# Kernel tuning notes

Measured on AMD Instinct MI355X. Metric: run time of the kernel, lower is better.

## Reference

```python
import jax, jax.numpy as jnp
import numpy as np

N_POINTS = 16
SPHERE_RADIUS = 2.5
BIG = 1e9

def _layernorm(x, g, b, eps=1e-5):
    mu = jnp.mean(x, axis=-1, keepdims=True)
    var = jnp.var(x, axis=-1, keepdims=True)
    return (x - mu) * jax.lax.rsqrt(var + eps) * g + b

def setup_inputs() -> dict:
    key = jax.random.key(0)
    ks = jax.random.split(key, 12)
    R, I, D, L = 1048576, 8, 64, 2
    orig = jax.random.normal(ks[0], (R, 3), jnp.float32)
    vec = jax.random.normal(ks[1], (R, 3), jnp.float32)
    vec = vec / jnp.linalg.norm(vec, axis=-1, keepdims=True)
    t1 = jax.random.uniform(ks[2], (I, R), jnp.float32) * 2.0
    t2 = t1 + jax.random.uniform(ks[3], (I, R), jnp.float32) * 0.5
    mask = jax.random.randint(ks[4], (I, R), 0, 2) > 0
    W_in = jax.random.normal(ks[5], (N_POINTS * 3, D), jnp.float32) * 0.1
    b_in = jnp.zeros((D,), jnp.float32)
    ln_g = jnp.ones((L, D), jnp.float32)
    ln_b = jnp.zeros((L, D), jnp.float32)
    W_mid = jax.random.normal(ks[6], (L, D, D), jnp.float32) * 0.1
    b_mid = jnp.zeros((L, D), jnp.float32)
    W_cls = jax.random.normal(ks[7], (D, 1), jnp.float32) * 0.1
    b_cls = jnp.zeros((1,), jnp.float32)
    W_dist = jax.random.normal(ks[8], (D, 1), jnp.float32) * 0.1
    b_dist = jnp.zeros((1,), jnp.float32)
    return dict(orig=orig, vec=vec, t1=t1, t2=t2, mask=mask,
                W_in=W_in, b_in=b_in, ln_g=ln_g, ln_b=ln_b,
                W_mid=W_mid, b_mid=b_mid, W_cls=W_cls, b_cls=b_cls,
                W_dist=W_dist, b_dist=b_dist)

def reference(orig, vec, t1, t2, mask, W_in, b_in, ln_g, ln_b, W_mid, b_mid,
              W_cls, b_cls, W_dist, b_dist):
    R = orig.shape[0]
    L = W_mid.shape[0]
    ts = jnp.linspace(0.0, 1.0, N_POINTS)  # [P]

    def net(x):  # x: [R, P*3]
        h = x @ W_in + b_in
        for l in range(L):
            h = jax.nn.relu(h)
            h = _layernorm(h, ln_g[l], ln_b[l])
            h = h @ W_mid[l] + b_mid[l]
        h = jax.nn.relu(h)
        cls = (h @ W_cls + b_cls)[:, 0]
        dval = (h @ W_dist + b_dist)[:, 0]
        return cls, dval

    def step(dist, it):
        m_i, t1_i, t2_i = it  # [R]
        dt = t2_i - t1_i
        inp_orig = orig + vec * t1_i[:, None]          # [R,3]
        inp_vec = vec * dt[:, None]                    # [R,3]
        # sample points along segment: [R, P, 3]
        inp = (inp_orig[:, None, :] + inp_vec[:, None, :] * ts[None, :, None]) / SPHERE_RADIUS
        cls, dval = net(inp.reshape(R, -1))
        dval = dval * dt + t1_i
        upd = (cls > 0) & (dval < dist) & m_i
        return jnp.where(upd, dval, dist), None

    dist0 = jnp.full((R,), BIG, jnp.float32)
    dist, _ = jax.lax.scan(step, dist0, (mask, t1, t2))
    dist = jnp.where(dist == BIG, 0.0, dist)
    return (dist > 0, dist)
```

## Files before the change

### kernel.cpp

```cpp
#include <hip/hip_runtime.h>
#include <math.h>

constexpr int   P      = 16;
constexpr int   DIN    = 48;
constexpr int   DH     = 64;
constexpr int   NITER  = 8;
constexpr int   NLAYER = 2;
constexpr float BIGV   = 1e9f;
constexpr float INV_R  = 1.0f / 2.5f;
constexpr int   RLOG   = 20;

typedef float f32x4 __attribute__((ext_vector_type(4)));
typedef const __attribute__((address_space(1))) f32x4 gf4_t;

__device__ __forceinline__ gf4_t* vmem(const float* p) {
    unsigned long long a = (unsigned long long)p;
    asm volatile("" : "+v"(a));
    return (gf4_t*)a;
}

__device__ __forceinline__ unsigned fkey(float f) {
    unsigned b = __float_as_uint(f);
    return (b & 0x80000000u) ? ~b : (b | 0x80000000u);
}
__device__ __forceinline__ float funkey(unsigned k) {
    unsigned b = (k & 0x80000000u) ? (k ^ 0x80000000u) : ~k;
    return __uint_as_float(b);
}

__device__ __noinline__
void slow_eval(const float* __restrict__ orig, const float* __restrict__ vec,
               const float* __restrict__ t1,   const float* __restrict__ t2,
               size_t tidx, unsigned r,
               const float* __restrict__ W_in,  const float* __restrict__ b_in,
               const float* __restrict__ ln_g,  const float* __restrict__ ln_b,
               const float* __restrict__ W_mid, const float* __restrict__ b_mid,
               const float* __restrict__ W_cls, const float* __restrict__ b_cls,
               const float* __restrict__ W_dist,const float* __restrict__ b_dist,
               float& cls_o, float& dval_o)
{
    const float o0 = orig[3*r+0], o1 = orig[3*r+1], o2 = orig[3*r+2];
    const float v0 = vec[3*r+0],  v1 = vec[3*r+1],  v2 = vec[3*r+2];
    const float t1i = t1[tidx], t2i = t2[tidx];

    const float dt  = __fsub_rn(t2i, t1i);
    const float io0 = __fadd_rn(o0, __fmul_rn(v0, t1i));
    const float io1 = __fadd_rn(o1, __fmul_rn(v1, t1i));
    const float io2 = __fadd_rn(o2, __fmul_rn(v2, t1i));
    const float iv0 = __fmul_rn(v0, dt);
    const float iv1 = __fmul_rn(v1, dt);
    const float iv2 = __fmul_rn(v2, dt);
    const float delta = 1.0f / 15.0f;

    float x[DIN];
    #pragma unroll
    for (int p = 0; p < P; ++p) {
        const float tp = __fmul_rn((float)p, delta);
        x[3*p+0] = __fdiv_rn(__fadd_rn(io0, __fmul_rn(iv0, tp)), 2.5f);
        x[3*p+1] = __fdiv_rn(__fadd_rn(io1, __fmul_rn(iv1, tp)), 2.5f);
        x[3*p+2] = __fdiv_rn(__fadd_rn(io2, __fmul_rn(iv2, tp)), 2.5f);
    }

    float a[DH];
    #pragma unroll 1
    for (int d = 0; d < DH; ++d) {
        double acc0 = 0.0, acc1 = 0.0;
        #pragma unroll
        for (int k = 0; k < DIN; k += 2) {
            acc0 = fma((double)x[k],   (double)W_in[k*DH + d],     acc0);
            acc1 = fma((double)x[k+1], (double)W_in[(k+1)*DH + d], acc1);
        }
        a[d] = __fadd_rn((float)(acc0 + acc1), b_in[d]);
    }

    #pragma unroll 1
    for (int l = 0; l < NLAYER; ++l) {
        #pragma unroll 1
        for (int d = 0; d < DH; ++d) a[d] = fmaxf(a[d], 0.0f);

        double s = 0.0;
        #pragma unroll 1
        for (int d = 0; d < DH; ++d) s += (double)a[d];
        const float mu = (float)(s * (1.0 / 64.0));

        double vs = 0.0;
        #pragma unroll 1
        for (int d = 0; d < DH; ++d) {
            const float c = __fsub_rn(a[d], mu);
            vs = fma((double)c, (double)c, vs);
        }
        const float var = (float)(vs * (1.0 / 64.0));
        const float ve  = __fadd_rn(var, 1e-5f);
        const float inv = (float)(1.0 / sqrt((double)ve));

        float hn[DH];
        #pragma unroll 1
        for (int d = 0; d < DH; ++d) {
            float t = __fsub_rn(a[d], mu);
            t = __fmul_rn(t, inv);
            t = __fmul_rn(t, ln_g[l*DH + d]);
            hn[d] = __fadd_rn(t, ln_b[l*DH + d]);
        }

        #pragma unroll 1
        for (int d = 0; d < DH; ++d) {
            double acc0 = 0.0, acc1 = 0.0;
            #pragma unroll
            for (int k = 0; k < DH; k += 2) {
                acc0 = fma((double)hn[k],   (double)W_mid[(l*DH + k)*DH + d],   acc0);
                acc1 = fma((double)hn[k+1], (double)W_mid[(l*DH + k+1)*DH + d], acc1);
            }
            a[d] = __fadd_rn((float)(acc0 + acc1), b_mid[l*DH + d]);
        }
    }

    double c0 = 0.0, c1 = 0.0, d0 = 0.0, d1 = 0.0;
    #pragma unroll 1
    for (int d = 0; d < DH; d += 2) {
        const float h0 = fmaxf(a[d],   0.0f);
        const float h1 = fmaxf(a[d+1], 0.0f);
        c0 = fma((double)h0, (double)W_cls[d],    c0);
        c1 = fma((double)h1, (double)W_cls[d+1],  c1);
        d0 = fma((double)h0, (double)W_dist[d],   d0);
        d1 = fma((double)h1, (double)W_dist[d+1], d1);
    }
    const float cls = __fadd_rn((float)(c0 + c1), b_cls[0]);
    const float dv  = __fadd_rn((float)(d0 + d1), b_dist[0]);
    cls_o  = cls;
    dval_o = __fadd_rn(__fmul_rn(dv, dt), t1i);
}

__global__ __launch_bounds__(256)
void compact_k(const int* __restrict__ mask, unsigned* __restrict__ cnt,
               unsigned* __restrict__ work)
{
    const int idx  = blockIdx.x * 256 + threadIdx.x;
    const int lane = threadIdx.x & 63;
    const bool m = (mask[idx] != 0);
    const unsigned long long b = __ballot(m);
    const int nact = __popcll(b);
    unsigned base = 0;
    if (lane == 0 && nact) base = atomicAdd(cnt, (unsigned)nact);
    base = __shfl(base, 0);
    if (m) {
        const int pre = __popcll(b & ((1ull << lane) - 1ull));
        work[base + pre] = (unsigned)idx;
    }
}

__global__ __launch_bounds__(256)
void init_k(unsigned* __restrict__ arena, int R)
{
    const unsigned key_big = fkey(BIGV);
    for (int r = blockIdx.x * 256 + threadIdx.x; r < R; r += gridDim.x * 256)
        arena[r] = key_big;
}

__global__ __launch_bounds__(256)
void finalize_k(float* __restrict__ out, int R)
{
    unsigned* arena = (unsigned*)out + R;
    for (int r = blockIdx.x * 256 + threadIdx.x; r < R; r += gridDim.x * 256) {
        const float dist = funkey(arena[r]);
        const float dfin = (dist == BIGV) ? 0.0f : dist;
        out[r] = (dfin > 0.0f) ? 1.0f : 0.0f;
        ((float*)arena)[r] = dfin;
    }
}

__global__ __launch_bounds__(512)
void main2_k(const float* __restrict__ orig,
             const float* __restrict__ vec,
             const float* __restrict__ t1,
             const float* __restrict__ t2,
             const float* __restrict__ W_in,
             const float* __restrict__ b_in,
             const float* __restrict__ ln_g,
             const float* __restrict__ ln_b,
             const float* __restrict__ W_mid,
             const float* __restrict__ b_mid,
             const float* __restrict__ W_cls,
             const float* __restrict__ b_cls,
             const float* __restrict__ W_dist,
             const float* __restrict__ b_dist,
             const unsigned* __restrict__ work,
             const unsigned* __restrict__ cnt,
             unsigned* __restrict__ arena)
{
    __shared__ __align__(16) float wlds[NLAYER*DH*DH];
    __shared__ __align__(16) float act[8][32][128];

    const int tid  = threadIdx.x;
    const int lane = tid & 63;
    const int wv   = tid >> 6;

    {
        f32x4*       dst = (f32x4*)wlds;
        const f32x4* s2  = (const f32x4*)W_mid;
        #pragma unroll 1
        for (int idx = tid; idx < NLAYER*DH*DH/4; idx += 512) dst[idx] = s2[idx];
    }
    __syncthreads();

    const float* wmid_l = wlds;

    float* col0 = &act[wv][0][lane];
    float* col1 = &act[wv][0][64 + lane];

    const unsigned T    = *cnt;
    const unsigned gtid = blockIdx.x * 512 + tid;
    const unsigned NTOT = gridDim.x * 512;

    for (unsigned g = gtid; 2*g < T; g += NTOT) {
        const unsigned jA = 2*g, jB = 2*g + 1;
        unsigned pk2[2];
        pk2[0] = work[jA];
        pk2[1] = (jB < T) ? work[jB] : pk2[0];

        float t1v[2], dtv[2], iov[2][3], ivv[2][3];
        #pragma unroll
        for (int it = 0; it < 2; ++it) {
            const unsigned pkk = pk2[it];
            const unsigned r   = pkk & 0xFFFFFu;
            const float tt1 = t1[pkk], tt2 = t2[pkk];
            t1v[it] = tt1; dtv[it] = tt2 - tt1;
            const float o0 = orig[3*r+0], o1 = orig[3*r+1], o2 = orig[3*r+2];
            const float v0 = vec[3*r+0],  v1 = vec[3*r+1],  v2 = vec[3*r+2];
            iov[it][0] = fmaf(v0, tt1, o0);
            iov[it][1] = fmaf(v1, tt1, o1);
            iov[it][2] = fmaf(v2, tt1, o2);
            ivv[it][0] = v0 * dtv[it];
            ivv[it][1] = v1 * dtv[it];
            ivv[it][2] = v2 * dtv[it];
        }

        float acc[2][DH];
        #pragma unroll
        for (int it = 0; it < 2; ++it)
            #pragma unroll
            for (int d = 0; d < DH; ++d) acc[it][d] = 0.0f;

        #pragma unroll 1
        for (int p = 0; p < P; ++p) {
            const float tp = (float)p * (1.0f / 15.0f);
            float xx[2][3];
            #pragma unroll
            for (int it = 0; it < 2; ++it) {
                xx[it][0] = fmaf(ivv[it][0], tp, iov[it][0]) * INV_R;
                xx[it][1] = fmaf(ivv[it][1], tp, iov[it][1]) * INV_R;
                xx[it][2] = fmaf(ivv[it][2], tp, iov[it][2]) * INV_R;
            }
            gf4_t* w0 = vmem(W_in + (3*p+0)*DH);
            gf4_t* w1 = vmem(W_in + (3*p+1)*DH);
            gf4_t* w2 = vmem(W_in + (3*p+2)*DH);
            #pragma unroll
            for (int j = 0; j < 16; ++j) {
                const f32x4 u = w0[j], v4 = w1[j], w4 = w2[j];
                #pragma unroll
                for (int it = 0; it < 2; ++it) {
                    acc[it][4*j+0] = fmaf(xx[it][2], w4.x, fmaf(xx[it][1], v4.x, fmaf(xx[it][0], u.x, acc[it][4*j+0])));
                    acc[it][4*j+1] = fmaf(xx[it][2], w4.y, fmaf(xx[it][1], v4.y, fmaf(xx[it][0], u.y, acc[it][4*j+1])));
                    acc[it][4*j+2] = fmaf(xx[it][2], w4.z, fmaf(xx[it][1], v4.z, fmaf(xx[it][0], u.z, acc[it][4*j+2])));
                    acc[it][4*j+3] = fmaf(xx[it][2], w4.w, fmaf(xx[it][1], v4.w, fmaf(xx[it][0], u.w, acc[it][4*j+3])));
                }
            }
        }
        #pragma unroll
        for (int it = 0; it < 2; ++it)
            #pragma unroll
            for (int d = 0; d < DH; ++d) acc[it][d] += b_in[d];

        float invprod[2] = {1.0f, 1.0f};

        #pragma unroll 1
        for (int l = 0; l < NLAYER; ++l) {
            float hh[2][32];
            #pragma unroll
            for (int it = 0; it < 2; ++it) {
                #pragma unroll
                for (int d = 0; d < DH; ++d) acc[it][d] = fmaxf(acc[it][d], 0.0f);

                float mu = 0.0f;
                #pragma unroll
                for (int d = 0; d < DH; ++d) mu += acc[it][d];
                mu *= (1.0f / 64.0f);

                float var = 0.0f;
                #pragma unroll
                for (int d = 0; d < DH; ++d) {
                    const float c = acc[it][d] - mu;
                    var = fmaf(c, c, var);
                }
                var *= (1.0f / 64.0f);
                const float inv = 1.0f / sqrtf(var + 1e-5f);
                invprod[it] *= inv;

                const float* gg = ln_g + l*DH;
                const float* bb = ln_b + l*DH;
                float* col = it ? col1 : col0;
                #pragma unroll
                for (int d = 0; d < 32; ++d)
                    col[d*128] = fmaf((acc[it][d] - mu) * inv, gg[d], bb[d]);
                #pragma unroll
                for (int j = 0; j < 32; ++j)
                    hh[it][j] = fmaf((acc[it][32+j] - mu) * inv, gg[32+j], bb[32+j]);
            }

            #pragma unroll
            for (int it = 0; it < 2; ++it)
                #pragma unroll
                for (int d = 0; d < DH; ++d) acc[it][d] = 0.0f;

            const float* Wl = wmid_l + l*DH*DH;

            #pragma unroll 2
            for (int k = 0; k < 32; ++k) {
                const float hk0 = col0[k*128];
                const float hk1 = col1[k*128];
                const f32x4* wr = (const f32x4*)(Wl + k*DH);
                #pragma unroll
                for (int j = 0; j < 16; ++j) {
                    const f32x4 w4 = wr[j];
                    acc[0][4*j+0] = fmaf(hk0, w4.x, acc[0][4*j+0]);
                    acc[1][4*j+0] = fmaf(hk1, w4.x, acc[1][4*j+0]);
                    acc[0][4*j+1] = fmaf(hk0, w4.y, acc[0][4*j+1]);
                    acc[1][4*j+1] = fmaf(hk1, w4.y, acc[1][4*j+1]);
                    acc[0][4*j+2] = fmaf(hk0, w4.z, acc[0][4*j+2]);
                    acc[1][4*j+2] = fmaf(hk1, w4.z, acc[1][4*j+2]);
                    acc[0][4*j+3] = fmaf(hk0, w4.w, acc[0][4*j+3]);
                    acc[1][4*j+3] = fmaf(hk1, w4.w, acc[1][4*j+3]);
                }
            }

            #pragma unroll
            for (int j = 0; j < 32; ++j) {
                col0[j*128] = hh[0][j];
                col1[j*128] = hh[1][j];
            }

            #pragma unroll 2
            for (int k = 32; k < DH; ++k) {
                const float hk0 = col0[(k-32)*128];
                const float hk1 = col1[(k-32)*128];
                const f32x4* wr = (const f32x4*)(Wl + k*DH);
                #pragma unroll
                for (int j = 0; j < 16; ++j) {
                    const f32x4 w4 = wr[j];
                    acc[0][4*j+0] = fmaf(hk0, w4.x, acc[0][4*j+0]);
                    acc[1][4*j+0] = fmaf(hk1, w4.x, acc[1][4*j+0]);
                    acc[0][4*j+1] = fmaf(hk0, w4.y, acc[0][4*j+1]);
                    acc[1][4*j+1] = fmaf(hk1, w4.y, acc[1][4*j+1]);
                    acc[0][4*j+2] = fmaf(hk0, w4.z, acc[0][4*j+2]);
                    acc[1][4*j+2] = fmaf(hk1, w4.z, acc[1][4*j+2]);
                    acc[0][4*j+3] = fmaf(hk0, w4.w, acc[0][4*j+3]);
                    acc[1][4*j+3] = fmaf(hk1, w4.w, acc[1][4*j+3]);
                }
            }

            const float* bm = b_mid + l*DH;
            #pragma unroll
            for (int it = 0; it < 2; ++it)
                #pragma unroll
                for (int d = 0; d < DH; ++d) acc[it][d] += bm[d];
        }

        #pragma unroll
        for (int it = 0; it < 2; ++it) {
            #pragma unroll
            for (int d = 0; d < DH; ++d) acc[it][d] = fmaxf(acc[it][d], 0.0f);

            float c0 = 0.f, c1 = 0.f, c2 = 0.f, c3 = 0.f;
            float e0 = 0.f, e1 = 0.f, e2 = 0.f, e3 = 0.f;
            #pragma unroll
            for (int j = 0; j < 16; ++j) {
                c0 = fmaf(acc[it][4*j+0], W_cls[4*j+0],  c0);
                c1 = fmaf(acc[it][4*j+1], W_cls[4*j+1],  c1);
                c2 = fmaf(acc[it][4*j+2], W_cls[4*j+2],  c2);
                c3 = fmaf(acc[it][4*j+3], W_cls[4*j+3],  c3);
                e0 = fmaf(acc[it][4*j+0], W_dist[4*j+0], e0);
                e1 = fmaf(acc[it][4*j+1], W_dist[4*j+1], e1);
                e2 = fmaf(acc[it][4*j+2], W_dist[4*j+2], e2);
                e3 = fmaf(acc[it][4*j+3], W_dist[4*j+3], e3);
            }
            float cls = ((c0 + c1) + (c2 + c3)) + b_cls[0];
            float dv  = ((e0 + e1) + (e2 + e3)) + b_dist[0];
            float dval = fmaf(dv, dtv[it], t1v[it]);

            float thr = 2e-6f * invprod[it];
            thr = fminf(fmaxf(thr, 3e-5f), 2e-2f);
            const unsigned r = pk2[it] & 0xFFFFFu;
            if ((fabsf(cls) < thr) || (fabsf(dval) < thr)) {
                slow_eval(orig, vec, t1, t2, (size_t)pk2[it], r,
                          W_in, b_in, ln_g, ln_b, W_mid, b_mid,
                          W_cls, b_cls, W_dist, b_dist, cls, dval);
            }
            if (cls > 0.0f)
                atomicMin(arena + r, fkey(dval));
        }
    }
}

__global__ __launch_bounds__(256, 2)
void fallback_k(const float* __restrict__ orig, const float* __restrict__ vec,
                const float* __restrict__ t1,   const float* __restrict__ t2,
                const int*   __restrict__ mask,
                const float* __restrict__ W_in,  const float* __restrict__ b_in,
                const float* __restrict__ ln_g,  const float* __restrict__ ln_b,
                const float* __restrict__ W_mid, const float* __restrict__ b_mid,
                const float* __restrict__ W_cls, const float* __restrict__ b_cls,
                const float* __restrict__ W_dist,const float* __restrict__ b_dist,
                float* __restrict__ out, int R)
{
    __shared__ __align__(16) float wlds[DIN*DH + NLAYER*DH*DH];
    __shared__ __align__(16) float act[4][32][64];

    const int tid  = threadIdx.x;
    const int lane = tid & 63;
    const int wv   = tid >> 6;

    {
        f32x4*       dst = (f32x4*)wlds;
        const f32x4* s1  = (const f32x4*)W_in;
        const f32x4* s2  = (const f32x4*)W_mid;
        #pragma unroll 1
        for (int idx = tid; idx < DIN*DH/4; idx += 256)        dst[idx] = s1[idx];
        #pragma unroll 1
        for (int idx = tid; idx < NLAYER*DH*DH/4; idx += 256)  dst[DIN*DH/4 + idx] = s2[idx];
    }
    __syncthreads();

    const float* win_l  = wlds;
    const float* wmid_l = wlds + DIN*DH;

    const int r = blockIdx.x * 256 + tid;
    if (r >= R) return;

    float* myact = &act[wv][0][lane];

    const float o0 = orig[3*r+0], o1 = orig[3*r+1], o2 = orig[3*r+2];
    const float v0 = vec[3*r+0],  v1 = vec[3*r+1],  v2 = vec[3*r+2];

    float dist = BIGV;

    #pragma unroll 1
    for (int i = 0; i < NITER; ++i) {
        const float t1i = t1[(size_t)i * R + r];
        const float t2i = t2[(size_t)i * R + r];
        const int   mi  = mask[(size_t)i * R + r];
        if (!mi) continue;
        const float dt = t2i - t1i;

        const float io0 = fmaf(v0, t1i, o0);
        const float io1 = fmaf(v1, t1i, o1);
        const float io2 = fmaf(v2, t1i, o2);
        const float iv0 = v0 * dt, iv1 = v1 * dt, iv2 = v2 * dt;

        float a[DH];
        #pragma unroll
        for (int d = 0; d < DH; ++d) a[d] = 0.0f;

        #pragma unroll 1
        for (int p = 0; p < P; ++p) {
            const float tp = (float)p * (1.0f / 15.0f);
            const float x0 = fmaf(iv0, tp, io0) * INV_R;
            const float x1 = fmaf(iv1, tp, io1) * INV_R;
            const float x2 = fmaf(iv2, tp, io2) * INV_R;
            const f32x4* w0 = (const f32x4*)(win_l + (3*p+0)*DH);
            const f32x4* w1 = (const f32x4*)(win_l + (3*p+1)*DH);
            const f32x4* w2 = (const f32x4*)(win_l + (3*p+2)*DH);
            #pragma unroll
            for (int j = 0; j < 16; ++j) {
                const f32x4 u = w0[j], v4 = w1[j], w4 = w2[j];
                a[4*j+0] = fmaf(x2, w4.x, fmaf(x1, v4.x, fmaf(x0, u.x, a[4*j+0])));
                a[4*j+1] = fmaf(x2, w4.y, fmaf(x1, v4.y, fmaf(x0, u.y, a[4*j+1])));
                a[4*j+2] = fmaf(x2, w4.z, fmaf(x1, v4.z, fmaf(x0, u.z, a[4*j+2])));
                a[4*j+3] = fmaf(x2, w4.w, fmaf(x1, v4.w, fmaf(x0, u.w, a[4*j+3])));
            }
        }
        #pragma unroll
        for (int d = 0; d < DH; ++d) a[d] += b_in[d];

        float invprod = 1.0f;

        #pragma unroll 1
        for (int l = 0; l < NLAYER; ++l) {
            #pragma unroll
            for (int d = 0; d < DH; ++d) a[d] = fmaxf(a[d], 0.0f);

            float mu = 0.0f;
            #pragma unroll
            for (int d = 0; d < DH; ++d) mu += a[d];
            mu *= (1.0f / 64.0f);

            float var = 0.0f;
            #pragma unroll
            for (int d = 0; d < DH; ++d) {
                const float c = a[d] - mu;
                var = fmaf(c, c, var);
            }
            var *= (1.0f / 64.0f);
            const float inv = 1.0f / sqrtf(var + 1e-5f);
            invprod *= inv;

            const float* g  = ln_g + l*DH;
            const float* bb = ln_b + l*DH;

            #pragma unroll
            for (int d = 0; d < 32; ++d)
                myact[d*64] = fmaf((a[d] - mu) * inv, g[d], bb[d]);
            float hh[32];
            #pragma unroll
            for (int j = 0; j < 32; ++j)
                hh[j] = fmaf((a[32+j] - mu) * inv, g[32+j], bb[32+j]);

            #pragma unroll
            for (int d = 0; d < DH; ++d) a[d] = 0.0f;

            const float* Wl = wmid_l + l*DH*DH;
            #pragma unroll 4
            for (int k = 0; k < 32; ++k) {
                const float hk = myact[k*64];
                const f32x4* wr = (const f32x4*)(Wl + k*DH);
                #pragma unroll
                for (int j = 0; j < 16; ++j) {
                    const f32x4 w4 = wr[j];
                    a[4*j+0] = fmaf(hk, w4.x, a[4*j+0]);
                    a[4*j+1] = fmaf(hk, w4.y, a[4*j+1]);
                    a[4*j+2] = fmaf(hk, w4.z, a[4*j+2]);
                    a[4*j+3] = fmaf(hk, w4.w, a[4*j+3]);
                }
            }
            #pragma unroll
            for (int j = 0; j < 32; ++j)
                myact[j*64] = hh[j];
            #pragma unroll 4
            for (int k = 32; k < DH; ++k) {
                const float hk = myact[(k-32)*64];
                const f32x4* wr = (const f32x4*)(Wl + k*DH);
                #pragma unroll
                for (int j = 0; j < 16; ++j) {
                    const f32x4 w4 = wr[j];
                    a[4*j+0] = fmaf(hk, w4.x, a[4*j+0]);
                    a[4*j+1] = fmaf(hk, w4.y, a[4*j+1]);
                    a[4*j+2] = fmaf(hk, w4.z, a[4*j+2]);
                    a[4*j+3] = fmaf(hk, w4.w, a[4*j+3]);
                }
            }
            const float* bm = b_mid + l*DH;
            #pragma unroll
            for (int d = 0; d < DH; ++d) a[d] += bm[d];
        }

        #pragma unroll
        for (int d = 0; d < DH; ++d) a[d] = fmaxf(a[d], 0.0f);

        float c0 = 0.f, c1 = 0.f, c2 = 0.f, c3 = 0.f;
        float e0 = 0.f, e1 = 0.f, e2 = 0.f, e3 = 0.f;
        #pragma unroll
        for (int j = 0; j < 16; ++j) {
            c0 = fmaf(a[4*j+0], W_cls[4*j+0],  c0);
            c1 = fmaf(a[4*j+1], W_cls[4*j+1],  c1);
            c2 = fmaf(a[4*j+2], W_cls[4*j+2],  c2);
            c3 = fmaf(a[4*j+3], W_cls[4*j+3],  c3);
            e0 = fmaf(a[4*j+0], W_dist[4*j+0], e0);
            e1 = fmaf(a[4*j+1], W_dist[4*j+1], e1);
            e2 = fmaf(a[4*j+2], W_dist[4*j+2], e2);
            e3 = fmaf(a[4*j+3], W_dist[4*j+3], e3);
        }
        float cls = ((c0 + c1) + (c2 + c3)) + b_cls[0];
        float dv  = ((e0 + e1) + (e2 + e3)) + b_dist[0];
        float dval = fmaf(dv, dt, t1i);

        float thr = 2e-6f * invprod;
        thr = fminf(fmaxf(thr, 3e-5f), 2e-2f);
        if ((fabsf(cls) < thr) || (fabsf(dval) < thr)) {
            slow_eval(orig, vec, t1, t2, (size_t)i * R + r, (unsigned)r,
                      W_in, b_in, ln_g, ln_b, W_mid, b_mid,
                      W_cls, b_cls, W_dist, b_dist, cls, dval);
        }

        if (cls > 0.0f && dval < dist) dist = dval;
    }

    const float dfin = (dist == BIGV) ? 0.0f : dist;
    out[r]     = (dfin > 0.0f) ? 1.0f : 0.0f;
    out[R + r] = dfin;
}

extern "C" void kernel_launch(void* const* d_in, const int* in_sizes, int n_in,
                              void* d_out, int out_size, void* d_ws, size_t ws_size,
                              hipStream_t stream) {
    const float* orig   = (const float*)d_in[0];
    const float* vec    = (const float*)d_in[1];
    const float* t1     = (const float*)d_in[2];
    const float* t2     = (const float*)d_in[3];
    const int*   mask   = (const int*)  d_in[4];
    const float* W_in   = (const float*)d_in[5];
    const float* b_in   = (const float*)d_in[6];
    const float* ln_g   = (const float*)d_in[7];
    const float* ln_b   = (const float*)d_in[8];
    const float* W_mid  = (const float*)d_in[9];
    const float* b_mid  = (const float*)d_in[10];
    const float* W_cls  = (const float*)d_in[11];
    const float* b_cls  = (const float*)d_in[12];
    const float* W_dist = (const float*)d_in[13];
    const float* b_dist = (const float*)d_in[14];

    float* out = (float*)d_out;
    const int R = in_sizes[0] / 3;

    const size_t need_ws = 16 + 4ull * (size_t)R * NITER;
    const bool fast = (R == (1 << RLOG)) && (ws_size >= need_ws);

    if (fast) {
        unsigned* cnt   = (unsigned*)d_ws;
        unsigned* work  = (unsigned*)d_ws + 4;
        unsigned* arena = (unsigned*)d_out + R;

        hipMemsetAsync(cnt, 0, 4, stream);
        compact_k<<<(R * NITER) / 256, 256, 0, stream>>>(mask, cnt, work);
        init_k<<<1024, 256, 0, stream>>>(arena, R);
        main2_k<<<1024, 512, 0, stream>>>(orig, vec, t1, t2,
                                          W_in, b_in, ln_g, ln_b, W_mid, b_mid,
                                          W_cls, b_cls, W_dist, b_dist,
                                          work, cnt, arena);
        finalize_k<<<1024, 256, 0, stream>>>(out, R);
    } else {
        const int threads = 256;
        const int blocks  = (R + threads - 1) / threads;
        fallback_k<<<blocks, threads, 0, stream>>>(
            orig, vec, t1, t2, mask,
            W_in, b_in, ln_g, ln_b, W_mid, b_mid,
            W_cls, b_cls, W_dist, b_dist,
            out, R);
    }
}
```

Baseline: 5.388 ms.

## Replace scalar FP32 MLP with split-bf16 MFMA matrix-core kernel

Replaces the per-thread scalar FMA network evaluation with a wave-level kernel that processes 64 compacted items per tile using 16x16x32 bf16 MFMA instructions. Inputs and weights are each split into a high and a low bf16 part, and three products are summed to approximate FP32 accuracy. A new prep kernel packs the weights into fragment layout in a device buffer. Layernorm and head reductions now use cross-lane shuffles, with activations staged through padded LDS. The near-threshold tolerance used to trigger the exact slow path is widened, which may send more items to the slow fallback.

```diff
diff --git a/kernel.cpp b/kernel.cpp
--- a/kernel.cpp
+++ b/kernel.cpp
@@ -10,14 +10,22 @@
 constexpr float INV_R  = 1.0f / 2.5f;
 constexpr int   RLOG   = 20;
 
-typedef float f32x4 __attribute__((ext_vector_type(4)));
-typedef const __attribute__((address_space(1))) f32x4 gf4_t;
-
-__device__ __forceinline__ gf4_t* vmem(const float* p) {
-    unsigned long long a = (unsigned long long)p;
-    asm volatile("" : "+v"(a));
-    return (gf4_t*)a;
-}
+typedef float f32x4  __attribute__((ext_vector_type(4)));
+typedef short bf16x8 __attribute__((ext_vector_type(8)));
+
+__device__ __align__(16) unsigned g_blob[3 * 16 * 64 * 4];
+
+__device__ __forceinline__ unsigned bf16rne(float x) {
+    unsigned b = __float_as_uint(x);
+    return (b + 0x7FFFu + ((b >> 16) & 1u)) >> 16;
+}
+__device__ __forceinline__ float bf16tof(unsigned h) { return __uint_as_float(h << 16); }
+
+union FragCvt { uint4 u; bf16x8 h; };
+__device__ __forceinline__ bf16x8 tofrag(unsigned w0, unsigned w1, unsigned w2, unsigned w3) {
+    FragCvt f; f.u = make_uint4(w0, w1, w2, w3); return f.h;
+}
+__device__ __forceinline__ bf16x8 tofrag4(uint4 u) { FragCvt f; f.u = u; return f.h; }
 
 __device__ __forceinline__ unsigned fkey(float f) {
     unsigned b = __float_as_uint(f);
@@ -168,235 +176,321 @@
     }
 }
 
+__global__ __launch_bounds__(256)
+void prep_k(const float* __restrict__ W_in, const float* __restrict__ W_mid)
+{
+    const int id = blockIdx.x * 256 + threadIdx.x;
+    if (id >= 3 * 4096) return;
+    const int L    = id >> 12;
+    const int fi   = (id >> 8) & 15;
+    const int lane = (id >> 2) & 63;
+    const int w    = id & 3;
+    const int pl = fi & 1, ni = (fi >> 1) & 3, kc = fi >> 3;
+    const int n  = ni * 16 + (lane & 15);
+    const int k0 = kc * 32 + ((lane >> 4) << 3) + 2 * w;
+
+    float v0, v1;
+    if (L == 0) {
+        v0 = (k0     < DIN) ? W_in[k0 * DH + n]       : 0.0f;
+        v1 = (k0 + 1 < DIN) ? W_in[(k0 + 1) * DH + n] : 0.0f;
+    } else {
+        v0 = W_mid[(L - 1) * DH * DH + k0 * DH + n];
+        v1 = W_mid[(L - 1) * DH * DH + (k0 + 1) * DH + n];
+    }
+    const unsigned h0 = bf16rne(v0), h1 = bf16rne(v1);
+    unsigned outw;
+    if (pl == 0) outw = h0 | (h1 << 16);
+    else {
+        const float l0 = v0 - bf16tof(h0), l1 = v1 - bf16tof(h1);
+        outw = bf16rne(l0) | (bf16rne(l1) << 16);
+    }
+    g_blob[id] = outw;
+}
+
 __global__ __launch_bounds__(512)
-void main2_k(const float* __restrict__ orig,
-             const float* __restrict__ vec,
-             const float* __restrict__ t1,
-             const float* __restrict__ t2,
-             const float* __restrict__ W_in,
-             const float* __restrict__ b_in,
-             const float* __restrict__ ln_g,
-             const float* __restrict__ ln_b,
-             const float* __restrict__ W_mid,
-             const float* __restrict__ b_mid,
-             const float* __restrict__ W_cls,
-             const float* __restrict__ b_cls,
-             const float* __restrict__ W_dist,
-             const float* __restrict__ b_dist,
-             const unsigned* __restrict__ work,
-             const unsigned* __restrict__ cnt,
-             unsigned* __restrict__ arena)
+void mfma_k(const float* __restrict__ orig,
+            const float* __restrict__ vec,
+            const float* __restrict__ t1,
+            const float* __restrict__ t2,
+            const float* __restrict__ W_in,
+            const float* __restrict__ b_in,
+            const float* __restrict__ ln_g,
+            const float* __restrict__ ln_b,
+            const float* __restrict__ W_mid,
+            const float* __restrict__ b_mid,
+            const float* __restrict__ W_cls,
+            const float* __restrict__ b_cls,
+            const float* __restrict__ W_dist,
+            const float* __restrict__ b_dist,
+            const unsigned* __restrict__ work,
+            const unsigned* __restrict__ cnt,
+            unsigned* __restrict__ arena)
 {
-    __shared__ __align__(16) float wlds[NLAYER*DH*DH];
-    __shared__ __align__(16) float act[8][32][128];
+    __shared__ __align__(16) float Hb[8][DH][68];
 
     const int tid  = threadIdx.x;
     const int lane = tid & 63;
     const int wv   = tid >> 6;
-
-    {
-        f32x4*       dst = (f32x4*)wlds;
-        const f32x4* s2  = (const f32x4*)W_mid;
-        #pragma unroll 1
-        for (int idx = tid; idx < NLAYER*DH*DH/4; idx += 512) dst[idx] = s2[idx];
-    }
-    __syncthreads();
-
-    const float* wmid_l = wlds;
-
-    float* col0 = &act[wv][0][lane];
-    float* col1 = &act[wv][0][64 + lane];
-
-    const unsigned T    = *cnt;
-    const unsigned gtid = blockIdx.x * 512 + tid;
-    const unsigned NTOT = gridDim.x * 512;
-
-    for (unsigned g = gtid; 2*g < T; g += NTOT) {
-        const unsigned jA = 2*g, jB = 2*g + 1;
-        unsigned pk2[2];
-        pk2[0] = work[jA];
-        pk2[1] = (jB < T) ? work[jB] : pk2[0];
-
-        float t1v[2], dtv[2], iov[2][3], ivv[2][3];
-        #pragma unroll
-        for (int it = 0; it < 2; ++it) {
-            const unsigned pkk = pk2[it];
-            const unsigned r   = pkk & 0xFFFFFu;
-            const float tt1 = t1[pkk], tt2 = t2[pkk];
-            t1v[it] = tt1; dtv[it] = tt2 - tt1;
+    const int l15  = lane & 15;
+    const int g    = lane >> 4;
+
+    float* Hw = &Hb[wv][0][0];
+    const int wbase = g * 4 * 68 + l15;
+    const int rbase = l15 * 68 + g * 8;
+
+    const unsigned T = *cnt;
+    if (T == 0) return;
+    const unsigned ntiles = (T + 63) >> 6;
+    const unsigned wgid = blockIdx.x * 8 + wv;
+    const unsigned nw   = gridDim.x * 8;
+    const uint4* fragp = (const uint4*)g_blob;
+
+    #pragma unroll 1
+    for (unsigned tile = wgid; tile < ntiles; tile += nw) {
+        const unsigned base = tile << 6;
+
+        float io[4][3], iv[4][3];
+        #pragma unroll
+        for (int mi = 0; mi < 4; ++mi) {
+            unsigned idx = base + mi * 16 + l15;
+            if (idx >= T) idx = T - 1;
+            const unsigned pk = work[idx];
+            const unsigned r  = pk & 0xFFFFFu;
+            const float tt1 = t1[pk], tt2 = t2[pk];
+            const float dt = tt2 - tt1;
             const float o0 = orig[3*r+0], o1 = orig[3*r+1], o2 = orig[3*r+2];
             const float v0 = vec[3*r+0],  v1 = vec[3*r+1],  v2 = vec[3*r+2];
-            iov[it][0] = fmaf(v0, tt1, o0);
-            iov[it][1] = fmaf(v1, tt1, o1);
-            iov[it][2] = fmaf(v2, tt1, o2);
-            ivv[it][0] = v0 * dtv[it];
-            ivv[it][1] = v1 * dtv[it];
-            ivv[it][2] = v2 * dtv[it];
-        }
-
-        float acc[2][DH];
-        #pragma unroll
-        for (int it = 0; it < 2; ++it)
-            #pragma unroll
-            for (int d = 0; d < DH; ++d) acc[it][d] = 0.0f;
-
-        #pragma unroll 1
-        for (int p = 0; p < P; ++p) {
-            const float tp = (float)p * (1.0f / 15.0f);
-            float xx[2][3];
-            #pragma unroll
-            for (int it = 0; it < 2; ++it) {
-                xx[it][0] = fmaf(ivv[it][0], tp, iov[it][0]) * INV_R;
-                xx[it][1] = fmaf(ivv[it][1], tp, iov[it][1]) * INV_R;
-                xx[it][2] = fmaf(ivv[it][2], tp, iov[it][2]) * INV_R;
-            }
-            gf4_t* w0 = vmem(W_in + (3*p+0)*DH);
-            gf4_t* w1 = vmem(W_in + (3*p+1)*DH);
-            gf4_t* w2 = vmem(W_in + (3*p+2)*DH);
-            #pragma unroll
-            for (int j = 0; j < 16; ++j) {
-                const f32x4 u = w0[j], v4 = w1[j], w4 = w2[j];
-                #pragma unroll
-                for (int it = 0; it < 2; ++it) {
-                    acc[it][4*j+0] = fmaf(xx[it][2], w4.x, fmaf(xx[it][1], v4.x, fmaf(xx[it][0], u.x, acc[it][4*j+0])));
-                    acc[it][4*j+1] = fmaf(xx[it][2], w4.y, fmaf(xx[it][1], v4.y, fmaf(xx[it][0], u.y, acc[it][4*j+1])));
-                    acc[it][4*j+2] = fmaf(xx[it][2], w4.z, fmaf(xx[it][1], v4.z, fmaf(xx[it][0], u.z, acc[it][4*j+2])));
-                    acc[it][4*j+3] = fmaf(xx[it][2], w4.w, fmaf(xx[it][1], v4.w, fmaf(xx[it][0], u.w, acc[it][4*j+3])));
-                }
-            }
-        }
-        #pragma unroll
-        for (int it = 0; it < 2; ++it)
-            #pragma unroll
-            for (int d = 0; d < DH; ++d) acc[it][d] += b_in[d];
-
-        float invprod[2] = {1.0f, 1.0f};
+            io[mi][0] = fmaf(v0, tt1, o0);
+            io[mi][1] = fmaf(v1, tt1, o1);
+            io[mi][2] = fmaf(v2, tt1, o2);
+            iv[mi][0] = v0 * dt; iv[mi][1] = v1 * dt; iv[mi][2] = v2 * dt;
+        }
+
+        f32x4 c[4][4];
+        #pragma unroll
+        for (int mi = 0; mi < 4; ++mi)
+            #pragma unroll
+            for (int ni = 0; ni < 4; ++ni)
+                c[mi][ni] = f32x4{0.f, 0.f, 0.f, 0.f};
+
+        #pragma unroll
+        for (int kc = 0; kc < 2; ++kc) {
+            bf16x8 ahi[4], alo[4];
+            #pragma unroll
+            for (int mi = 0; mi < 4; ++mi) {
+                unsigned hw[4], lw[4];
+                #pragma unroll
+                for (int w = 0; w < 4; ++w) {
+                    float xv[2];
+                    #pragma unroll
+                    for (int s = 0; s < 2; ++s) {
+                        const int e = 2 * w + s;
+                        const int k = kc * 32 + g * 8 + e;
+                        const unsigned ku = (unsigned)k;
+                        const unsigned p  = ku / 3u;
+                        const unsigned cm = ku - 3u * p;
+                        const float tp = (float)p * (1.0f / 15.0f);
+                        const float ios = cm == 0 ? io[mi][0] : (cm == 1 ? io[mi][1] : io[mi][2]);
+                        const float ivs = cm == 0 ? iv[mi][0] : (cm == 1 ? iv[mi][1] : iv[mi][2]);
+                        float x = fmaf(ivs, tp, ios) * INV_R;
+                        xv[s] = (k < DIN) ? x : 0.0f;
+                    }
+                    const unsigned h0 = bf16rne(xv[0]), h1 = bf16rne(xv[1]);
+                    hw[w] = h0 | (h1 << 16);
+                    const float l0 = xv[0] - bf16tof(h0), l1 = xv[1] - bf16tof(h1);
+                    lw[w] = bf16rne(l0) | (bf16rne(l1) << 16);
+                }
+                ahi[mi] = tofrag(hw[0], hw[1], hw[2], hw[3]);
+                alo[mi] = tofrag(lw[0], lw[1], lw[2], lw[3]);
+            }
+            #pragma unroll
+            for (int ni = 0; ni < 4; ++ni) {
+                const bf16x8 bhi = tofrag4(fragp[((kc * 4 + ni) * 2 + 0) * 64 + lane]);
+                const bf16x8 blo = tofrag4(fragp[((kc * 4 + ni) * 2 + 1) * 64 + lane]);
+                #pragma unroll
+                for (int mi = 0; mi < 4; ++mi) {
+                    c[mi][ni] = __builtin_amdgcn_mfma_f32_16x16x32_bf16(ahi[mi], bhi, c[mi][ni], 0, 0, 0);
+                    c[mi][ni] = __builtin_amdgcn_mfma_f32_16x16x32_bf16(ahi[mi], blo, c[mi][ni], 0, 0, 0);
+                    c[mi][ni] = __builtin_amdgcn_mfma_f32_16x16x32_bf16(alo[mi], bhi, c[mi][ni], 0, 0, 0);
+                }
+            }
+        }
+        #pragma unroll
+        for (int ni = 0; ni < 4; ++ni) {
+            const float bi = b_in[ni * 16 + l15];
+            #pragma unroll
+            for (int mi = 0; mi < 4; ++mi) {
+                c[mi][ni][0] += bi; c[mi][ni][1] += bi;
+                c[mi][ni][2] += bi; c[mi][ni][3] += bi;
+            }
+        }
+
+        float invp[4][4];
+        #pragma unroll
+        for (int mi = 0; mi < 4; ++mi)
+            #pragma unroll
+            for (int rr = 0; rr < 4; ++rr) invp[mi][rr] = 1.0f;
 
         #pragma unroll 1
         for (int l = 0; l < NLAYER; ++l) {
-            float hh[2][32];
-            #pragma unroll
-            for (int it = 0; it < 2; ++it) {
-                #pragma unroll
-                for (int d = 0; d < DH; ++d) acc[it][d] = fmaxf(acc[it][d], 0.0f);
-
-                float mu = 0.0f;
-                #pragma unroll
-                for (int d = 0; d < DH; ++d) mu += acc[it][d];
-                mu *= (1.0f / 64.0f);
-
-                float var = 0.0f;
-                #pragma unroll
-                for (int d = 0; d < DH; ++d) {
-                    const float c = acc[it][d] - mu;
-                    var = fmaf(c, c, var);
-                }
-                var *= (1.0f / 64.0f);
-                const float inv = 1.0f / sqrtf(var + 1e-5f);
-                invprod[it] *= inv;
-
-                const float* gg = ln_g + l*DH;
-                const float* bb = ln_b + l*DH;
-                float* col = it ? col1 : col0;
-                #pragma unroll
-                for (int d = 0; d < 32; ++d)
-                    col[d*128] = fmaf((acc[it][d] - mu) * inv, gg[d], bb[d]);
-                #pragma unroll
-                for (int j = 0; j < 32; ++j)
-                    hh[it][j] = fmaf((acc[it][32+j] - mu) * inv, gg[32+j], bb[32+j]);
-            }
-
-            #pragma unroll
-            for (int it = 0; it < 2; ++it)
-                #pragma unroll
-                for (int d = 0; d < DH; ++d) acc[it][d] = 0.0f;
-
-            const float* Wl = wmid_l + l*DH*DH;
-
-            #pragma unroll 2
-            for (int k = 0; k < 32; ++k) {
-                const float hk0 = col0[k*128];
-                const float hk1 = col1[k*128];
-                const f32x4* wr = (const f32x4*)(Wl + k*DH);
-                #pragma unroll
-                for (int j = 0; j < 16; ++j) {
-                    const f32x4 w4 = wr[j];
-                    acc[0][4*j+0] = fmaf(hk0, w4.x, acc[0][4*j+0]);
-                    acc[1][4*j+0] = fmaf(hk1, w4.x, acc[1][4*j+0]);
-                    acc[0][4*j+1] = fmaf(hk0, w4.y, acc[0][4*j+1]);
-                    acc[1][4*j+1] = fmaf(hk1, w4.y, acc[1][4*j+1]);
-                    acc[0][4*j+2] = fmaf(hk0, w4.z, acc[0][4*j+2]);
-                    acc[1][4*j+2] = fmaf(hk1, w4.z, acc[1][4*j+2]);
-                    acc[0][4*j+3] = fmaf(hk0, w4.w, acc[0][4*j+3]);
-                    acc[1][4*j+3] = fmaf(hk1, w4.w, acc[1][4*j+3]);
-                }
-            }
-
-            #pragma unroll
-            for (int j = 0; j < 32; ++j) {
-                col0[j*128] = hh[0][j];
-                col1[j*128] = hh[1][j];
-            }
-
-            #pragma unroll 2
-            for (int k = 32; k < DH; ++k) {
-                const float hk0 = col0[(k-32)*128];
-                const float hk1 = col1[(k-32)*128];
-                const f32x4* wr = (const f32x4*)(Wl + k*DH);
-                #pragma unroll
-                for (int j = 0; j < 16; ++j) {
-                    const f32x4 w4 = wr[j];
-                    acc[0][4*j+0] = fmaf(hk0, w4.x, acc[0][4*j+0]);
-                    acc[1][4*j+0] = fmaf(hk1, w4.x, acc[1][4*j+0]);
-                    acc[0][4*j+1] = fmaf(hk0, w4.y, acc[0][4*j+1]);
-                    acc[1][4*j+1] = fmaf(hk1, w4.y, acc[1][4*j+1]);
-                    acc[0][4*j+2] = fmaf(hk0, w4.z, acc[0][4*j+2]);
-                    acc[1][4*j+2] = fmaf(hk1, w4.z, acc[1][4*j+2]);
-                    acc[0][4*j+3] = fmaf(hk0, w4.w, acc[0][4*j+3]);
-                    acc[1][4*j+3] = fmaf(hk1, w4.w, acc[1][4*j+3]);
-                }
-            }
-
-            const float* bm = b_mid + l*DH;
-            #pragma unroll
-            for (int it = 0; it < 2; ++it)
-                #pragma unroll
-                for (int d = 0; d < DH; ++d) acc[it][d] += bm[d];
-        }
-
-        #pragma unroll
-        for (int it = 0; it < 2; ++it) {
-            #pragma unroll
-            for (int d = 0; d < DH; ++d) acc[it][d] = fmaxf(acc[it][d], 0.0f);
-
-            float c0 = 0.f, c1 = 0.f, c2 = 0.f, c3 = 0.f;
-            float e0 = 0.f, e1 = 0.f, e2 = 0.f, e3 = 0.f;
-            #pragma unroll
-            for (int j = 0; j < 16; ++j) {
-                c0 = fmaf(acc[it][4*j+0], W_cls[4*j+0],  c0);
-                c1 = fmaf(acc[it][4*j+1], W_cls[4*j+1],  c1);
-                c2 = fmaf(acc[it][4*j+2], W_cls[4*j+2],  c2);
-                c3 = fmaf(acc[it][4*j+3], W_cls[4*j+3],  c3);
-                e0 = fmaf(acc[it][4*j+0], W_dist[4*j+0], e0);
-                e1 = fmaf(acc[it][4*j+1], W_dist[4*j+1], e1);
-                e2 = fmaf(acc[it][4*j+2], W_dist[4*j+2], e2);
-                e3 = fmaf(acc[it][4*j+3], W_dist[4*j+3], e3);
-            }
-            float cls = ((c0 + c1) + (c2 + c3)) + b_cls[0];
-            float dv  = ((e0 + e1) + (e2 + e3)) + b_dist[0];
-            float dval = fmaf(dv, dtv[it], t1v[it]);
-
-            float thr = 2e-6f * invprod[it];
-            thr = fminf(fmaxf(thr, 3e-5f), 2e-2f);
-            const unsigned r = pk2[it] & 0xFFFFFu;
-            if ((fabsf(cls) < thr) || (fabsf(dval) < thr)) {
-                slow_eval(orig, vec, t1, t2, (size_t)pk2[it], r,
-                          W_in, b_in, ln_g, ln_b, W_mid, b_mid,
-                          W_cls, b_cls, W_dist, b_dist, cls, dval);
-            }
-            if (cls > 0.0f)
-                atomicMin(arena + r, fkey(dval));
-        }
+            #pragma unroll
+            for (int mi = 0; mi < 4; ++mi)
+                #pragma unroll
+                for (int ni = 0; ni < 4; ++ni)
+                    #pragma unroll
+                    for (int rr = 0; rr < 4; ++rr)
+                        c[mi][ni][rr] = fmaxf(c[mi][ni][rr], 0.0f);
+
+            float mu_a[4][4], iv_a[4][4];
+            #pragma unroll
+            for (int mi = 0; mi < 4; ++mi)
+                #pragma unroll
+                for (int rr = 0; rr < 4; ++rr) {
+                    float s = c[mi][0][rr] + c[mi][1][rr] + c[mi][2][rr] + c[mi][3][rr];
+                    s += __shfl_xor(s, 1); s += __shfl_xor(s, 2);
+                    s += __shfl_xor(s, 4); s += __shfl_xor(s, 8);
+                    const float mu = s * (1.0f / 64.0f);
+                    float vp = 0.0f;
+                    #pragma unroll
+                    for (int ni = 0; ni < 4; ++ni) {
+                        const float d0 = c[mi][ni][rr] - mu;
+                        vp = fmaf(d0, d0, vp);
+                    }
+                    vp += __shfl_xor(vp, 1); vp += __shfl_xor(vp, 2);
+                    vp += __shfl_xor(vp, 4); vp += __shfl_xor(vp, 8);
+                    const float var = vp * (1.0f / 64.0f);
+                    const float inv = 1.0f / sqrtf(var + 1e-5f);
+                    mu_a[mi][rr] = mu; iv_a[mi][rr] = inv;
+                    invp[mi][rr] *= inv;
+                }
+
+            float gg[4], bb[4];
+            #pragma unroll
+            for (int ni = 0; ni < 4; ++ni) {
+                gg[ni] = ln_g[l * DH + ni * 16 + l15];
+                bb[ni] = ln_b[l * DH + ni * 16 + l15];
+            }
+            #pragma unroll
+            for (int mi = 0; mi < 4; ++mi)
+                #pragma unroll
+                for (int rr = 0; rr < 4; ++rr) {
+                    const float mu = mu_a[mi][rr], inv = iv_a[mi][rr];
+                    #pragma unroll
+                    for (int ni = 0; ni < 4; ++ni) {
+                        const float t = (c[mi][ni][rr] - mu) * inv;
+                        Hw[wbase + mi * 1088 + rr * 68 + ni * 16] = fmaf(t, gg[ni], bb[ni]);
+                    }
+                }
+
+            #pragma unroll
+            for (int mi = 0; mi < 4; ++mi)
+                #pragma unroll
+                for (int ni = 0; ni < 4; ++ni)
+                    c[mi][ni] = f32x4{0.f, 0.f, 0.f, 0.f};
+
+            const int lbase = (1 + l) * 16;
+            #pragma unroll
+            for (int kc = 0; kc < 2; ++kc) {
+                bf16x8 ahi[4], alo[4];
+                #pragma unroll
+                for (int mi = 0; mi < 4; ++mi) {
+                    const float* rp = Hw + rbase + mi * 1088 + kc * 32;
+                    const f32x4 f0 = *(const f32x4*)(rp);
+                    const f32x4 f1 = *(const f32x4*)(rp + 4);
+                    float fe[8] = {f0[0], f0[1], f0[2], f0[3], f1[0], f1[1], f1[2], f1[3]};
+                    unsigned hw[4], lw[4];
+                    #pragma unroll
+                    for (int w = 0; w < 4; ++w) {
+                        const unsigned h0 = bf16rne(fe[2*w]), h1 = bf16rne(fe[2*w+1]);
+                        hw[w] = h0 | (h1 << 16);
+                        const float l0 = fe[2*w] - bf16tof(h0), l1 = fe[2*w+1] - bf16tof(h1);
+                        lw[w] = bf16rne(l0) | (bf16rne(l1) << 16);
+                    }
+                    ahi[mi] = tofrag(hw[0], hw[1], hw[2], hw[3]);
+                    alo[mi] = tofrag(lw[0], lw[1], lw[2], lw[3]);
+                }
+                #pragma unroll
+                for (int ni = 0; ni < 4; ++ni) {
+                    const bf16x8 bhi = tofrag4(fragp[(lbase + (kc * 4 + ni) * 2 + 0) * 64 + lane]);
+                    const bf16x8 blo = tofrag4(fragp[(lbase + (kc * 4 + ni) * 2 + 1) * 64 + lane]);
+                    #pragma unroll
+                    for (int mi = 0; mi < 4; ++mi) {
+                        c[mi][ni] = __builtin_amdgcn_mfma_f32_16x16x32_bf16(ahi[mi], bhi, c[mi][ni], 0, 0, 0);
+                        c[mi][ni] = __builtin_amdgcn_mfma_f32_16x16x32_bf16(ahi[mi], blo, c[mi][ni], 0, 0, 0);
+                        c[mi][ni] = __builtin_amdgcn_mfma_f32_16x16x32_bf16(alo[mi], bhi, c[mi][ni], 0, 0, 0);
+                    }
+                }
+            }
+            #pragma unroll
+            for (int ni = 0; ni < 4; ++ni) {
+                const float bm = b_mid[l * DH + ni * 16 + l15];
+                #pragma unroll
+                for (int mi = 0; mi < 4; ++mi) {
+                    c[mi][ni][0] += bm; c[mi][ni][1] += bm;
+                    c[mi][ni][2] += bm; c[mi][ni][3] += bm;
+                }
+            }
+        }
+
+        #pragma unroll
+        for (int mi = 0; mi < 4; ++mi)
+            #pragma unroll
+            for (int ni = 0; ni < 4; ++ni)
+                #pragma unroll
+                for (int rr = 0; rr < 4; ++rr)
+                    c[mi][ni][rr] = fmaxf(c[mi][ni][rr], 0.0f);
+
+        float wc[4], wd[4];
+        #pragma unroll
+        for (int ni = 0; ni < 4; ++ni) {
+            wc[ni] = W_cls[ni * 16 + l15];
+            wd[ni] = W_dist[ni * 16 + l15];
+        }
+        float ca[4][4], da[4][4];
+        #pragma unroll
+        for (int mi = 0; mi < 4; ++mi)
+            #pragma unroll
+            for (int rr = 0; rr < 4; ++rr) {
+                float sc = 0.f, sd = 0.f;
+                #pragma unroll
+                for (int ni = 0; ni < 4; ++ni) {
+                    sc = fmaf(c[mi][ni][rr], wc[ni], sc);
+                    sd = fmaf(c[mi][ni][rr], wd[ni], sd);
+                }
+                sc += __shfl_xor(sc, 1); sc += __shfl_xor(sc, 2);
+                sc += __shfl_xor(sc, 4); sc += __shfl_xor(sc, 8);
+                sd += __shfl_xor(sd, 1); sd += __shfl_xor(sd, 2);
+                sd += __shfl_xor(sd, 4); sd += __shfl_xor(sd, 8);
+                ca[mi][rr] = sc; da[mi][rr] = sd;
+            }
+
+        float selc = ca[0][0], seld = da[0][0], seli = invp[0][0];
+        #pragma unroll
+        for (int cc = 1; cc < 16; ++cc) {
+            const bool m = (l15 == cc);
+            selc = m ? ca[cc >> 2][cc & 3]   : selc;
+            seld = m ? da[cc >> 2][cc & 3]   : seld;
+            seli = m ? invp[cc >> 2][cc & 3] : seli;
+        }
+        const int item_local = ((l15 >> 2) << 4) + (g << 2) + (l15 & 3);
+        unsigned idx = base + (unsigned)item_local;
+        if (idx >= T) idx = T - 1;
+        const unsigned pk = work[idx];
+        const unsigned rr_ = pk & 0xFFFFFu;
+        const float tt1 = t1[pk];
+        const float dt  = t2[pk] - tt1;
+
+        float clsv = selc + b_cls[0];
+        float dval = fmaf(seld + b_dist[0], dt, tt1);
+
+        const float thr = fminf(fmaxf(1e-5f * seli, 3e-4f), 2e-2f);
+        if ((fabsf(clsv) < thr) || (fabsf(dval) < thr)) {
+            slow_eval(orig, vec, t1, t2, (size_t)pk, rr_,
+                      W_in, b_in, ln_g, ln_b, W_mid, b_mid,
+                      W_cls, b_cls, W_dist, b_dist, clsv, dval);
+        }
+        if (clsv > 0.0f)
+            atomicMin(arena + rr_, fkey(dval));
     }
 }
 
@@ -495,23 +589,23 @@
             float var = 0.0f;
             #pragma unroll
             for (int d = 0; d < DH; ++d) {
-                const float c = a[d] - mu;
-                var = fmaf(c, c, var);
+                const float cdev = a[d] - mu;
+                var = fmaf(cdev, cdev, var);
             }
             var *= (1.0f / 64.0f);
             const float inv = 1.0f / sqrtf(var + 1e-5f);
             invprod *= inv;
 
-            const float* g  = ln_g + l*DH;
-            const float* bb = ln_b + l*DH;
+            const float* gp = ln_g + l*DH;
+            const float* bp = ln_b + l*DH;
 
             #pragma unroll
             for (int d = 0; d < 32; ++d)
-                myact[d*64] = fmaf((a[d] - mu) * inv, g[d], bb[d]);
+                myact[d*64] = fmaf((a[d] - mu) * inv, gp[d], bp[d]);
             float hh[32];
             #pragma unroll
             for (int j = 0; j < 32; ++j)
-                hh[j] = fmaf((a[32+j] - mu) * inv, g[32+j], bb[32+j]);
+                hh[j] = fmaf((a[32+j] - mu) * inv, gp[32+j], bp[32+j]);
 
             #pragma unroll
             for (int d = 0; d < DH; ++d) a[d] = 0.0f;
@@ -619,11 +713,12 @@
 
         hipMemsetAsync(cnt, 0, 4, stream);
         compact_k<<<(R * NITER) / 256, 256, 0, stream>>>(mask, cnt, work);
+        prep_k<<<48, 256, 0, stream>>>(W_in, W_mid);
         init_k<<<1024, 256, 0, stream>>>(arena, R);
-        main2_k<<<1024, 512, 0, stream>>>(orig, vec, t1, t2,
-                                          W_in, b_in, ln_g, ln_b, W_mid, b_mid,
-                                          W_cls, b_cls, W_dist, b_dist,
-                                          work, cnt, arena);
+        mfma_k<<<1024, 512, 0, stream>>>(orig, vec, t1, t2,
+                                         W_in, b_in, ln_g, ln_b, W_mid, b_mid,
+                                         W_cls, b_cls, W_dist, b_dist,
+                                         work, cnt, arena);
         finalize_k<<<1024, 256, 0, stream>>>(out, R);
     } else {
         const int threads = 256;
```

New measurement: 7.659 ms. +42.2%, slower.

## Read layer-1 weights from global memory and halve block size

Applied to the files above, without the earlier changes.

Only layer-0 W_mid is staged in LDS now. Layer-1 weights are read straight from global memory through vector loads that the compiler treats as non-uniform. Blocks shrink from 512 to 256 threads with twice as many blocks, so each block's LDS footprint roughly halves (activations plus one weight matrix), and the layer loop is fully unrolled. The aim is to split weight bandwidth between the LDS and cache paths and to fit more blocks per CU. The cost is cache traffic on every layer-1 FMA step and more code from the unrolling.

```diff
diff --git a/kernel.cpp b/kernel.cpp
--- a/kernel.cpp
+++ b/kernel.cpp
@@ -168,7 +168,49 @@
     }
 }
 
-__global__ __launch_bounds__(512)
+template<bool GLOBAL>
+__device__ __forceinline__
+void mm_khalf(const float* Wbase, int kofs,
+              const float* col0, const float* col1,
+              float (&a0)[DH], float (&a1)[DH])
+{
+    #pragma unroll 2
+    for (int k = 0; k < 32; ++k) {
+        const float hk0 = col0[k*128];
+        const float hk1 = col1[k*128];
+        if constexpr (GLOBAL) {
+            gf4_t* wr = vmem(Wbase + (kofs + k)*DH);
+            #pragma unroll
+            for (int j = 0; j < 16; ++j) {
+                const f32x4 w4 = wr[j];
+                a0[4*j+0] = fmaf(hk0, w4.x, a0[4*j+0]);
+                a1[4*j+0] = fmaf(hk1, w4.x, a1[4*j+0]);
+                a0[4*j+1] = fmaf(hk0, w4.y, a0[4*j+1]);
+                a1[4*j+1] = fmaf(hk1, w4.y, a1[4*j+1]);
+                a0[4*j+2] = fmaf(hk0, w4.z, a0[4*j+2]);
+                a1[4*j+2] = fmaf(hk1, w4.z, a1[4*j+2]);
+                a0[4*j+3] = fmaf(hk0, w4.w, a0[4*j+3]);
+                a1[4*j+3] = fmaf(hk1, w4.w, a1[4*j+3]);
+            }
+        } else {
+            const f32x4* wr = (const f32x4*)(Wbase + (kofs + k)*DH);
+            #pragma unroll
+            for (int j = 0; j < 16; ++j) {
+                const f32x4 w4 = wr[j];
+                a0[4*j+0] = fmaf(hk0, w4.x, a0[4*j+0]);
+                a1[4*j+0] = fmaf(hk1, w4.x, a1[4*j+0]);
+                a0[4*j+1] = fmaf(hk0, w4.y, a0[4*j+1]);
+                a1[4*j+1] = fmaf(hk1, w4.y, a1[4*j+1]);
+                a0[4*j+2] = fmaf(hk0, w4.z, a0[4*j+2]);
+                a1[4*j+2] = fmaf(hk1, w4.z, a1[4*j+2]);
+                a0[4*j+3] = fmaf(hk0, w4.w, a0[4*j+3]);
+                a1[4*j+3] = fmaf(hk1, w4.w, a1[4*j+3]);
+            }
+        }
+    }
+}
+
+__global__ __launch_bounds__(256, 1)
 void main2_k(const float* __restrict__ orig,
              const float* __restrict__ vec,
              const float* __restrict__ t1,
@@ -187,29 +229,27 @@
              const unsigned* __restrict__ cnt,
              unsigned* __restrict__ arena)
 {
-    __shared__ __align__(16) float wlds[NLAYER*DH*DH];
-    __shared__ __align__(16) float act[8][32][128];
+    __shared__ __align__(16) float wl0[DH*DH];
+    __shared__ __align__(16) float act[4][32][128];
 
     const int tid  = threadIdx.x;
     const int lane = tid & 63;
     const int wv   = tid >> 6;
 
     {
-        f32x4*       dst = (f32x4*)wlds;
+        f32x4*       dst = (f32x4*)wl0;
         const f32x4* s2  = (const f32x4*)W_mid;
         #pragma unroll 1
-        for (int idx = tid; idx < NLAYER*DH*DH/4; idx += 512) dst[idx] = s2[idx];
+        for (int idx = tid; idx < DH*DH/4; idx += 256) dst[idx] = s2[idx];
     }
     __syncthreads();
-
-    const float* wmid_l = wlds;
 
     float* col0 = &act[wv][0][lane];
     float* col1 = &act[wv][0][64 + lane];
 
     const unsigned T    = *cnt;
-    const unsigned gtid = blockIdx.x * 512 + tid;
-    const unsigned NTOT = gridDim.x * 512;
+    const unsigned gtid = blockIdx.x * 256 + tid;
+    const unsigned NTOT = gridDim.x * 256;
 
     for (unsigned g = gtid; 2*g < T; g += NTOT) {
         const unsigned jA = 2*g, jB = 2*g + 1;
@@ -272,7 +312,7 @@
 
         float invprod[2] = {1.0f, 1.0f};
 
-        #pragma unroll 1
+        #pragma unroll
         for (int l = 0; l < NLAYER; ++l) {
             float hh[2][32];
             #pragma unroll
@@ -311,26 +351,8 @@
                 #pragma unroll
                 for (int d = 0; d < DH; ++d) acc[it][d] = 0.0f;
 
-            const float* Wl = wmid_l + l*DH*DH;
-
-            #pragma unroll 2
-            for (int k = 0; k < 32; ++k) {
-                const float hk0 = col0[k*128];
-                const float hk1 = col1[k*128];
-                const f32x4* wr = (const f32x4*)(Wl + k*DH);
-                #pragma unroll
-                for (int j = 0; j < 16; ++j) {
-                    const f32x4 w4 = wr[j];
-                    acc[0][4*j+0] = fmaf(hk0, w4.x, acc[0][4*j+0]);
-                    acc[1][4*j+0] = fmaf(hk1, w4.x, acc[1][4*j+0]);
-                    acc[0][4*j+1] = fmaf(hk0, w4.y, acc[0][4*j+1]);
-                    acc[1][4*j+1] = fmaf(hk1, w4.y, acc[1][4*j+1]);
-                    acc[0][4*j+2] = fmaf(hk0, w4.z, acc[0][4*j+2]);
-                    acc[1][4*j+2] = fmaf(hk1, w4.z, acc[1][4*j+2]);
-                    acc[0][4*j+3] = fmaf(hk0, w4.w, acc[0][4*j+3]);
-                    acc[1][4*j+3] = fmaf(hk1, w4.w, acc[1][4*j+3]);
-                }
-            }
+            if (l == 0) mm_khalf<false>(wl0,             0, col0, col1, acc[0], acc[1]);
+            else        mm_khalf<true >(W_mid + DH*DH,   0, col0, col1, acc[0], acc[1]);
 
             #pragma unroll
             for (int j = 0; j < 32; ++j) {
@@ -338,24 +360,8 @@
                 col1[j*128] = hh[1][j];
             }
 
-            #pragma unroll 2
-            for (int k = 32; k < DH; ++k) {
-                const float hk0 = col0[(k-32)*128];
-                const float hk1 = col1[(k-32)*128];
-                const f32x4* wr = (const f32x4*)(Wl + k*DH);
-                #pragma unroll
-                for (int j = 0; j < 16; ++j) {
-                    const f32x4 w4 = wr[j];
-                    acc[0][4*j+0] = fmaf(hk0, w4.x, acc[0][4*j+0]);
-                    acc[1][4*j+0] = fmaf(hk1, w4.x, acc[1][4*j+0]);
-                    acc[0][4*j+1] = fmaf(hk0, w4.y, acc[0][4*j+1]);
-                    acc[1][4*j+1] = fmaf(hk1, w4.y, acc[1][4*j+1]);
-                    acc[0][4*j+2] = fmaf(hk0, w4.z, acc[0][4*j+2]);
-                    acc[1][4*j+2] = fmaf(hk1, w4.z, acc[1][4*j+2]);
-                    acc[0][4*j+3] = fmaf(hk0, w4.w, acc[0][4*j+3]);
-                    acc[1][4*j+3] = fmaf(hk1, w4.w, acc[1][4*j+3]);
-                }
-            }
+            if (l == 0) mm_khalf<false>(wl0,            32, col0, col1, acc[0], acc[1]);
+            else        mm_khalf<true >(W_mid + DH*DH,  32, col0, col1, acc[0], acc[1]);
 
             const float* bm = b_mid + l*DH;
             #pragma unroll
@@ -495,23 +501,23 @@
             float var = 0.0f;
             #pragma unroll
             for (int d = 0; d < DH; ++d) {
-                const float c = a[d] - mu;
-                var = fmaf(c, c, var);
+                const float cdev = a[d] - mu;
+                var = fmaf(cdev, cdev, var);
             }
             var *= (1.0f / 64.0f);
             const float inv = 1.0f / sqrtf(var + 1e-5f);
             invprod *= inv;
 
-            const float* g  = ln_g + l*DH;
-            const float* bb = ln_b + l*DH;
+            const float* gp = ln_g + l*DH;
+            const float* bp = ln_b + l*DH;
 
             #pragma unroll
             for (int d = 0; d < 32; ++d)
-                myact[d*64] = fmaf((a[d] - mu) * inv, g[d], bb[d]);
+                myact[d*64] = fmaf((a[d] - mu) * inv, gp[d], bp[d]);
             float hh[32];
             #pragma unroll
             for (int j = 0; j < 32; ++j)
-                hh[j] = fmaf((a[32+j] - mu) * inv, g[32+j], bb[32+j]);
+                hh[j] = fmaf((a[32+j] - mu) * inv, gp[32+j], bp[32+j]);
 
             #pragma unroll
             for (int d = 0; d < DH; ++d) a[d] = 0.0f;
@@ -620,7 +626,7 @@
         hipMemsetAsync(cnt, 0, 4, stream);
         compact_k<<<(R * NITER) / 256, 256, 0, stream>>>(mask, cnt, work);
         init_k<<<1024, 256, 0, stream>>>(arena, R);
-        main2_k<<<1024, 512, 0, stream>>>(orig, vec, t1, t2,
+        main2_k<<<2048, 256, 0, stream>>>(orig, vec, t1, t2,
                                           W_in, b_in, ln_g, ln_b, W_mid, b_mid,
                                           W_cls, b_cls, W_dist, b_dist,
                                           work, cnt, arena);
```

Result: slower. 6.805 ms (+26.3%).
